# Optimization experiments

Hardware: AMD Instinct MI355X
Metric: run time of the kernel (lower is better)

## Reference

```python
import jax, jax.numpy as jnp
import numpy as np

N = 50000
IN_C = 128
HID = 128  # 2 * out_channels
OUT_C = 64
E = 800000


def setup_inputs() -> dict:
    key = jax.random.key(0)
    k1, k2, k3, k4, k5, k6 = jax.random.split(key, 6)
    x = jax.random.normal(k1, (N, IN_C), dtype=jnp.float32)
    edge_index = jax.random.randint(k2, (2, E), 0, N, dtype=jnp.int64)
    # Glorot init like PyG GCNConv
    W1 = jax.random.normal(k3, (IN_C, HID), dtype=jnp.float32) * np.sqrt(2.0 / (IN_C + HID))
    b1 = jnp.zeros((HID,), dtype=jnp.float32)
    W2 = jax.random.normal(k4, (HID, OUT_C), dtype=jnp.float32) * np.sqrt(2.0 / (HID + OUT_C))
    b2 = jnp.zeros((OUT_C,), dtype=jnp.float32)
    return {"x": x, "edge_index": edge_index, "W1": W1, "b1": b1, "W2": W2, "b2": b2}


def _gcn_norm(edge_index, num_nodes):
    # PyG gcn_norm with add_self_loops=True, edge_weight=1:
    # deg[i] = number of incoming edges to i (including self loop)
    # norm(e) = deg[src]^-0.5 * deg[dst]^-0.5
    loops = jnp.arange(num_nodes, dtype=edge_index.dtype)
    src = jnp.concatenate([edge_index[0], loops])
    dst = jnp.concatenate([edge_index[1], loops])
    deg = jax.ops.segment_sum(jnp.ones_like(dst, dtype=jnp.float32), dst,
                              num_segments=num_nodes)
    dinv = jnp.where(deg > 0, jax.lax.rsqrt(deg), 0.0)
    norm = dinv[src] * dinv[dst]
    return src, dst, norm


def _gcn_layer(x, W, b, src, dst, norm, num_nodes):
    h = x @ W                                    # [N, D_out] dense GEMM first (PyG order)
    msg = h[src] * norm[:, None]                 # gather + scale: [E+N, D_out]
    out = jax.ops.segment_sum(msg, dst, num_segments=num_nodes)  # scatter-add
    return out + b


def reference(x, edge_index, W1, b1, W2, b2):
    num_nodes = x.shape[0]
    # cached=True in the original: normalization computed once, reused by both convs
    src, dst, norm = _gcn_norm(edge_index, num_nodes)
    h = _gcn_layer(x, W1, b1, src, dst, norm, num_nodes)
    h = jax.nn.relu(h)
    out = _gcn_layer(h, W2, b2, src, dst, norm, num_nodes)
    return out
```

## Files before the change

### kernel.cpp

```cpp
#include <hip/hip_runtime.h>
#include <hip/hip_bf16.h>


typedef unsigned short ushort_t;
typedef __attribute__((ext_vector_type(8))) short bf16x8;
typedef __attribute__((ext_vector_type(4))) float f32x4;

__device__ __forceinline__ float blo(int v) {
    union { int i; float f; } u;
    u.i = v << 16;
    return u.f;
}

__device__ __forceinline__ float bhi(int v) {
    union { int i; float f; } u;
    u.i = v & 0xffff0000;
    return u.f;
}

__device__ __forceinline__ ushort_t f2bf(float f) {
    __hip_bfloat16 h = __float2bfloat16(f);
    return *reinterpret_cast<ushort_t*>(&h);
}

#define BMAX 512
#define CHUNK 2048
#define CAP 3072
#define NPH 8


__global__ __launch_bounds__(256) void gemm1bin_k(const float* __restrict__ X,
                                                  const float* __restrict__ W,
                                                  ushort_t* __restrict__ H,
                                                  const int* __restrict__ src,
                                                  const int* __restrict__ dst,
                                                  int* __restrict__ bucket_cursor,
                                                  int* __restrict__ binned,
                                                  int n, int E, int G1) {
    __shared__ __align__(16) char smem[52224];
    const int t = threadIdx.x;

    if ((int)blockIdx.x < G1) {
        ushort_t (*As)[136] = reinterpret_cast<ushort_t(*)[136]>(smem);
        ushort_t (*Bt)[136] = reinterpret_cast<ushort_t(*)[136]>(smem + 64 * 136 * 2);
        const int row0 = blockIdx.x * 64;
#pragma unroll
        for (int rep = 0; rep < 8; rep++) {
            int idx = rep * 1024 + t * 4;
            int r = idx >> 7, c = idx & 127;
            int gr = row0 + r;
            float4 v = make_float4(0.f, 0.f, 0.f, 0.f);
            if (gr < n) v = *reinterpret_cast<const float4*>(X + (size_t)gr * 128 + c);
            As[r][c + 0] = f2bf(v.x); As[r][c + 1] = f2bf(v.y);
            As[r][c + 2] = f2bf(v.z); As[r][c + 3] = f2bf(v.w);
        }
#pragma unroll
        for (int rep = 0; rep < 16; rep++) {
            int idx = rep * 1024 + t * 4;
            int k = idx >> 7, nn = idx & 127;
            float4 v = *reinterpret_cast<const float4*>(W + k * 128 + nn);
            Bt[nn + 0][k] = f2bf(v.x); Bt[nn + 1][k] = f2bf(v.y);
            Bt[nn + 2][k] = f2bf(v.z); Bt[nn + 3][k] = f2bf(v.w);
        }
        __syncthreads();
        const int lane = t & 63;
        const int wave = t >> 6;
        const int l15 = lane & 15;
        const int koff = (lane >> 4) * 8;
        f32x4 acc[8] = {};
#pragma unroll
        for (int ks = 0; ks < 4; ks++) {
            int kb = ks * 32 + koff;
            bf16x8 a = *reinterpret_cast<const bf16x8*>(&As[wave * 16 + l15][kb]);
#pragma unroll
            for (int tc = 0; tc < 8; tc++) {
                bf16x8 b = *reinterpret_cast<const bf16x8*>(&Bt[tc * 16 + l15][kb]);
                acc[tc] = __builtin_amdgcn_mfma_f32_16x16x32_bf16(a, b, acc[tc], 0, 0, 0);
            }
        }
        const int rbase = row0 + wave * 16 + (lane >> 4) * 4;
#pragma unroll
        for (int reg = 0; reg < 4; reg++) {
            int gr = rbase + reg;
            if (gr < n) {
#pragma unroll
                for (int tc = 0; tc < 8; tc++)
                    H[(size_t)gr * 128 + tc * 16 + l15] = f2bf(acc[tc][reg]);
            }
        }
    } else {
        int* lcnt = (int*)smem;
        int* lbase = lcnt + BMAX;
        int* lcur = lbase + BMAX;
        const int nchunks = (E + CHUNK - 1) / CHUNK;
        const int nbin = (int)gridDim.x - G1;
        for (int ch = (int)blockIdx.x - G1; ch < nchunks; ch += nbin) {
            int base = ch * CHUNK;
            int cnt = min(CHUNK, E - base);
            for (int i = t; i < BMAX; i += 256) lcnt[i] = 0;
            __syncthreads();
            for (int k = t; k < cnt; k += 256)
                atomicAdd(&lcnt[dst[base + k] >> 7], 1);
            __syncthreads();
            for (int i = t; i < BMAX; i += 256) {
                int c = lcnt[i];
                if (c) lbase[i] = atomicAdd(&bucket_cursor[i], c);
                lcur[i] = 0;
            }
            __syncthreads();
            for (int k = t; k < cnt; k += 256) {
                int d = dst[base + k];
                int b = d >> 7;
                int r = atomicAdd(&lcur[b], 1);
                int pos = lbase[b] + r;
                if (pos < CAP)
                    binned[b * CAP + pos] = (src[base + k] << 7) | (d & 127);
            }
            __syncthreads();
        }
    }
}

__global__ __launch_bounds__(256) void finalize_k(const int* __restrict__ binned,
                                                  const int* __restrict__ bucket_cursor,
                                                  float* __restrict__ dinv,
                                                  int2* __restrict__ row_range,
                                                  ushort_t* __restrict__ csr,
                                                  int N, int B) {
    __shared__ int cnt[128][NPH];
    __shared__ int sc[128];
    int b = blockIdx.x;
    int tid = threadIdx.x;
    int node0 = b << 7;
    int nn = min(128, N - node0);
    int e0 = b * CAP;
    int e1 = e0 + min(bucket_cursor[b], CAP);
    const int phw = (N + NPH - 1) / NPH;

    for (int i = tid; i < 128 * NPH; i += 256) ((int*)cnt)[i] = 0;
    __syncthreads();
    for (int k = e0 + tid; k < e1; k += 256) {
        int e = binned[k];
        int s = (int)((unsigned)e >> 7);
        atomicAdd(&cnt[e & 127][s / phw], 1);
    }
    __syncthreads();
    int deg = 0;
    int pre[NPH];
    if (tid < 128) {
#pragma unroll
        for (int p = 0; p < NPH; p++) { pre[p] = deg; deg += cnt[tid][p]; }
        sc[tid] = (tid < nn) ? deg : 0;
    }
    __syncthreads();
    for (int off = 1; off < 128; off <<= 1) {
        int t2 = 0;
        if (tid < 128 && tid >= off) t2 = sc[tid - off];
        __syncthreads();
        if (tid < 128) sc[tid] += t2;
        __syncthreads();
    }
    if (tid < nn) {
        int ex = sc[tid] - deg;
        int g = node0 + tid;
        dinv[g] = rsqrtf((float)deg + 1.0f);
        row_range[g] = make_int2(e0 + ex, e0 + ex + deg);
#pragma unroll
        for (int p = 0; p < NPH; p++) cnt[tid][p] = ex + pre[p];
    }
    __syncthreads();
    for (int k = e0 + tid; k < e1; k += 256) {
        int e = binned[k];
        int s = (int)((unsigned)e >> 7);
        int slot = atomicAdd(&cnt[e & 127][s / phw], 1);
        csr[e0 + slot] = (ushort_t)s;
    }
}


__global__ __launch_bounds__(256) void gemm2_k(const ushort_t* __restrict__ X,
                                               const float* __restrict__ W,
                                               const float* __restrict__ dinv,
                                               ushort_t* __restrict__ H, int n) {
    __shared__ ushort_t As[64][136];
    __shared__ ushort_t Bt[64][136];
    const int t = threadIdx.x;
    const int row0 = blockIdx.x * 64;
#pragma unroll
    for (int rep = 0; rep < 8; rep++) {
        int idx = rep * 1024 + t * 4;
        int r = idx >> 7, c = idx & 127;
        int gr = row0 + r;
        ushort4 v = make_ushort4(0, 0, 0, 0);
        if (gr < n) v = *reinterpret_cast<const ushort4*>(X + (size_t)gr * 128 + c);
        As[r][c + 0] = v.x; As[r][c + 1] = v.y; As[r][c + 2] = v.z; As[r][c + 3] = v.w;
    }
#pragma unroll
    for (int rep = 0; rep < 8; rep++) {
        int idx = rep * 1024 + t * 4;
        int k = idx >> 6, nn = idx & 63;
        float4 v = *reinterpret_cast<const float4*>(W + k * 64 + nn);
        Bt[nn + 0][k] = f2bf(v.x); Bt[nn + 1][k] = f2bf(v.y);
        Bt[nn + 2][k] = f2bf(v.z); Bt[nn + 3][k] = f2bf(v.w);
    }
    __syncthreads();
    const int lane = t & 63;
    const int wave = t >> 6;
    const int l15 = lane & 15;
    const int koff = (lane >> 4) * 8;
    f32x4 acc[4] = {};
#pragma unroll
    for (int ks = 0; ks < 4; ks++) {
        int kb = ks * 32 + koff;
        bf16x8 a = *reinterpret_cast<const bf16x8*>(&As[wave * 16 + l15][kb]);
#pragma unroll
        for (int tc = 0; tc < 4; tc++) {
            bf16x8 b = *reinterpret_cast<const bf16x8*>(&Bt[tc * 16 + l15][kb]);
            acc[tc] = __builtin_amdgcn_mfma_f32_16x16x32_bf16(a, b, acc[tc], 0, 0, 0);
        }
    }
    const int rbase = row0 + wave * 16 + (lane >> 4) * 4;
#pragma unroll
    for (int reg = 0; reg < 4; reg++) {
        int gr = rbase + reg;
        if (gr < n) {
            float dv = dinv[gr];
#pragma unroll
            for (int tc = 0; tc < 4; tc++)
                H[(size_t)gr * 64 + tc * 16 + l15] = f2bf(acc[tc][reg] * dv);
        }
    }
}

#define FMA8(VV, WT)                                                    \
    a0 = fmaf(blo((VV).x), (WT), a0); a1 = fmaf(bhi((VV).x), (WT), a1); \
    a2 = fmaf(blo((VV).y), (WT), a2); a3 = fmaf(bhi((VV).y), (WT), a3); \
    a4 = fmaf(blo((VV).z), (WT), a4); a5 = fmaf(bhi((VV).z), (WT), a5); \
    a6 = fmaf(blo((VV).w), (WT), a6); a7 = fmaf(bhi((VV).w), (WT), a7);


__global__ __launch_bounds__(256) void agg1_k(const ushort_t* __restrict__ h,
                                              const int2* __restrict__ row_range,
                                              const ushort_t* __restrict__ csr,
                                              const float* __restrict__ dinv,
                                              const float* __restrict__ bias,
                                              ushort_t* __restrict__ out, int n) {
    const int t = threadIdx.x;
    const int i = blockIdx.x * 16 + (t >> 4);
    if (i >= n) return;
    const int q = t & 15;
    const ushort_t* hq = h + 8 * q;
    float a0 = 0.f, a1 = 0.f, a2 = 0.f, a3 = 0.f;
    float a4 = 0.f, a5 = 0.f, a6 = 0.f, a7 = 0.f;
    const int2 rr = row_range[i];
    const int e = rr.y - 1;
    for (int j = rr.x; j < rr.y; j += 16) {
        int ss[16];
#pragma unroll
        for (int k = 0; k < 16; k++) ss[k] = (int)csr[min(j + k, e)];
        float ww[16];
#pragma unroll
        for (int k = 0; k < 16; k++) ww[k] = (j + k <= e) ? dinv[ss[k]] : 0.f;
#pragma unroll
        for (int k = 0; k < 16; k++) {
            int4 v = *reinterpret_cast<const int4*>(hq + (size_t)ss[k] * 128);
            FMA8(v, ww[k]);
        }
    }
    const float di = dinv[i];
    int4 sv = *reinterpret_cast<const int4*>(hq + (size_t)i * 128);
    FMA8(sv, di);
    float4 b0 = *reinterpret_cast<const float4*>(bias + 8 * q);
    float4 b1v = *reinterpret_cast<const float4*>(bias + 8 * q + 4);
    int4 o;
    o.x = (int)(((unsigned)f2bf(fmaxf(fmaf(di, a1, b0.y), 0.f)) << 16) | f2bf(fmaxf(fmaf(di, a0, b0.x), 0.f)));
    o.y = (int)(((unsigned)f2bf(fmaxf(fmaf(di, a3, b0.w), 0.f)) << 16) | f2bf(fmaxf(fmaf(di, a2, b0.z), 0.f)));
    o.z = (int)(((unsigned)f2bf(fmaxf(fmaf(di, a5, b1v.y), 0.f)) << 16) | f2bf(fmaxf(fmaf(di, a4, b1v.x), 0.f)));
    o.w = (int)(((unsigned)f2bf(fmaxf(fmaf(di, a7, b1v.w), 0.f)) << 16) | f2bf(fmaxf(fmaf(di, a6, b1v.z), 0.f)));
    *reinterpret_cast<int4*>(out + (size_t)i * 128 + 8 * q) = o;
}


__global__ __launch_bounds__(256) void agg2_k(const ushort_t* __restrict__ h,
                                              const int2* __restrict__ row_range,
                                              const ushort_t* __restrict__ csr,
                                              const float* __restrict__ dinv,
                                              const float* __restrict__ bias,
                                              float* __restrict__ out, int n) {
    const int t = threadIdx.x;
    const int i = blockIdx.x * 32 + (t >> 3);
    if (i >= n) return;
    const int q = t & 7;
    const ushort_t* hq = h + 8 * q;
    float a0 = 0.f, a1 = 0.f, a2 = 0.f, a3 = 0.f;
    float a4 = 0.f, a5 = 0.f, a6 = 0.f, a7 = 0.f;
    const int2 rr = row_range[i];
    const int e = rr.y - 1;
    for (int j = rr.x; j < rr.y; j += 16) {
        int ss[16];
#pragma unroll
        for (int k = 0; k < 16; k++) ss[k] = (int)csr[min(j + k, e)];
        float ww[16];
#pragma unroll
        for (int k = 0; k < 16; k++) ww[k] = (j + k <= e) ? 1.f : 0.f;
#pragma unroll
        for (int k = 0; k < 16; k++) {
            int4 v = *reinterpret_cast<const int4*>(hq + (size_t)ss[k] * 64);
            FMA8(v, ww[k]);
        }
    }
    int4 sv = *reinterpret_cast<const int4*>(hq + (size_t)i * 64);
    FMA8(sv, 1.f);
    const float di = dinv[i];
    float4 b0 = *reinterpret_cast<const float4*>(bias + 8 * q);
    float4 b1v = *reinterpret_cast<const float4*>(bias + 8 * q + 4);
    float4 o0 = make_float4(fmaf(di, a0, b0.x), fmaf(di, a1, b0.y),
                            fmaf(di, a2, b0.z), fmaf(di, a3, b0.w));
    float4 o1 = make_float4(fmaf(di, a4, b1v.x), fmaf(di, a5, b1v.y),
                            fmaf(di, a6, b1v.z), fmaf(di, a7, b1v.w));
    *reinterpret_cast<float4*>(out + (size_t)i * 64 + 8 * q) = o0;
    *reinterpret_cast<float4*>(out + (size_t)i * 64 + 8 * q + 4) = o1;
}


extern "C" void kernel_launch(void* const* d_in, const int* in_sizes, int n_in,
                              void* d_out, int out_size, void* d_ws, size_t ws_size,
                              hipStream_t stream) {
    const float* x   = (const float*)d_in[0];
    const int*   ei  = (const int*)d_in[1];
    const float* W1  = (const float*)d_in[2];
    const float* b1  = (const float*)d_in[3];
    const float* W2  = (const float*)d_in[4];
    const float* b2  = (const float*)d_in[5];
    float* out = (float*)d_out;

    const int N = in_sizes[0] / 128;
    const int E = in_sizes[1] / 2;
    const int B = (N + 127) >> 7;
    const int* src = ei;
    const int* dst = ei + E;

    char* p = (char*)d_ws;
    auto alloc = [&](size_t bytes) {
        char* q = p;
        p += (bytes + 255) & ~(size_t)255;
        return (void*)q;
    };
    int*      bucket_cursor = (int*)alloc((size_t)BMAX * 4);
    float*    dinv          = (float*)alloc((size_t)N * 4);
    int2*     row_range     = (int2*)alloc((size_t)N * 8);
    int*      binned        = (int*)alloc((size_t)B * CAP * 4);
    ushort_t* csr           = (ushort_t*)alloc(((size_t)B * CAP + 32) * 2);
    ushort_t* h1            = (ushort_t*)alloc((size_t)N * 128 * 2);
    ushort_t* agg1          = (ushort_t*)alloc((size_t)N * 128 * 2);
    ushort_t* h2            = h1;

    const int nchunks = (E + CHUNK - 1) / CHUNK;
    const int G1 = (N + 63) / 64;

    (void)hipMemsetAsync(bucket_cursor, 0, (size_t)B * 4, stream);
    gemm1bin_k<<<G1 + nchunks, 256, 0, stream>>>(x, W1, h1, src, dst,
                                                 bucket_cursor, binned, N, E, G1);
    finalize_k<<<B, 256, 0, stream>>>(binned, bucket_cursor, dinv, row_range, csr, N, B);

    agg1_k<<<(N + 15) / 16, 256, 0, stream>>>(h1, row_range, csr, dinv, b1, agg1, N);

    gemm2_k<<<(N + 63) / 64, 256, 0, stream>>>(agg1, W2, dinv, h2, N);
    agg2_k<<<(N + 31) / 32, 256, 0, stream>>>(h2, row_range, csr, dinv, b2, out, N);
}
```

Baseline: 185.6 us.

## Prescale layer-1 features by source dinv in finalize, drop per-edge dinv gather

The finalize kernel now multiplies each node's bf16 row of h1 by its own dinv after computing degrees, so agg1 no longer has to gather dinv[src] for every edge. Both aggregation kernels also replace the batched 16-wide index/weight prefetch with a simpler 8-wide unrolled loop. This removes one dependent random gather per edge in agg1, but adds a read-modify-write pass over h1 and an extra bf16 rounding step, and the smaller unroll may expose less memory-level parallelism.

```diff
diff --git a/kernel.cpp b/kernel.cpp
--- a/kernel.cpp
+++ b/kernel.cpp
@@ -21,6 +21,15 @@
 __device__ __forceinline__ ushort_t f2bf(float f) {
     __hip_bfloat16 h = __float2bfloat16(f);
     return *reinterpret_cast<ushort_t*>(&h);
+}
+
+__device__ __forceinline__ int4 scale8(int4 v, float s) {
+    int4 r;
+    r.x = (int)(((unsigned)f2bf(bhi(v.x) * s) << 16) | f2bf(blo(v.x) * s));
+    r.y = (int)(((unsigned)f2bf(bhi(v.y) * s) << 16) | f2bf(blo(v.y) * s));
+    r.z = (int)(((unsigned)f2bf(bhi(v.z) * s) << 16) | f2bf(blo(v.z) * s));
+    r.w = (int)(((unsigned)f2bf(bhi(v.w) * s) << 16) | f2bf(blo(v.w) * s));
+    return r;
 }
 
 #define BMAX 512
@@ -126,9 +135,11 @@
                                                   float* __restrict__ dinv,
                                                   int2* __restrict__ row_range,
                                                   ushort_t* __restrict__ csr,
+                                                  ushort_t* __restrict__ h1,
                                                   int N, int B) {
     __shared__ int cnt[128][NPH];
     __shared__ int sc[128];
+    __shared__ float sdv[128];
     int b = blockIdx.x;
     int tid = threadIdx.x;
     int node0 = b << 7;
@@ -160,13 +171,18 @@
         if (tid < 128) sc[tid] += t2;
         __syncthreads();
     }
-    if (tid < nn) {
-        int ex = sc[tid] - deg;
-        int g = node0 + tid;
-        dinv[g] = rsqrtf((float)deg + 1.0f);
-        row_range[g] = make_int2(e0 + ex, e0 + ex + deg);
-#pragma unroll
-        for (int p = 0; p < NPH; p++) cnt[tid][p] = ex + pre[p];
+    if (tid < 128) {
+        float dv = 0.f;
+        if (tid < nn) {
+            int ex = sc[tid] - deg;
+            int g = node0 + tid;
+            dv = rsqrtf((float)deg + 1.0f);
+            dinv[g] = dv;
+            row_range[g] = make_int2(e0 + ex, e0 + ex + deg);
+#pragma unroll
+            for (int p = 0; p < NPH; p++) cnt[tid][p] = ex + pre[p];
+        }
+        sdv[tid] = dv;
     }
     __syncthreads();
     for (int k = e0 + tid; k < e1; k += 256) {
@@ -174,6 +190,12 @@
         int s = (int)((unsigned)e >> 7);
         int slot = atomicAdd(&cnt[e & 127][s / phw], 1);
         csr[e0 + slot] = (ushort_t)s;
+    }
+    int4* h4 = reinterpret_cast<int4*>(h1);
+    for (int idx = tid; idx < nn * 16; idx += 256) {
+        int r = idx >> 4, c = idx & 15;
+        size_t off = (size_t)(node0 + r) * 16 + c;
+        h4[off] = scale8(h4[off], sdv[r]);
     }
 }
 
@@ -254,22 +276,19 @@
     float a4 = 0.f, a5 = 0.f, a6 = 0.f, a7 = 0.f;
     const int2 rr = row_range[i];
     const int e = rr.y - 1;
-    for (int j = rr.x; j < rr.y; j += 16) {
-        int ss[16];
-#pragma unroll
-        for (int k = 0; k < 16; k++) ss[k] = (int)csr[min(j + k, e)];
-        float ww[16];
-#pragma unroll
-        for (int k = 0; k < 16; k++) ww[k] = (j + k <= e) ? dinv[ss[k]] : 0.f;
-#pragma unroll
-        for (int k = 0; k < 16; k++) {
-            int4 v = *reinterpret_cast<const int4*>(hq + (size_t)ss[k] * 128);
-            FMA8(v, ww[k]);
+    for (int j = rr.x; j < rr.y; j += 8) {
+#pragma unroll
+        for (int k = 0; k < 8; k++) {
+            int jk = min(j + k, e);
+            int s = (int)csr[jk];
+            float w = (j + k <= e) ? 1.f : 0.f;
+            int4 v = *reinterpret_cast<const int4*>(hq + (size_t)s * 128);
+            FMA8(v, w);
         }
     }
     const float di = dinv[i];
     int4 sv = *reinterpret_cast<const int4*>(hq + (size_t)i * 128);
-    FMA8(sv, di);
+    FMA8(sv, 1.f);
     float4 b0 = *reinterpret_cast<const float4*>(bias + 8 * q);
     float4 b1v = *reinterpret_cast<const float4*>(bias + 8 * q + 4);
     int4 o;
@@ -296,17 +315,14 @@
     float a4 = 0.f, a5 = 0.f, a6 = 0.f, a7 = 0.f;
     const int2 rr = row_range[i];
     const int e = rr.y - 1;
-    for (int j = rr.x; j < rr.y; j += 16) {
-        int ss[16];
-#pragma unroll
-        for (int k = 0; k < 16; k++) ss[k] = (int)csr[min(j + k, e)];
-        float ww[16];
-#pragma unroll
-        for (int k = 0; k < 16; k++) ww[k] = (j + k <= e) ? 1.f : 0.f;
-#pragma unroll
-        for (int k = 0; k < 16; k++) {
-            int4 v = *reinterpret_cast<const int4*>(hq + (size_t)ss[k] * 64);
-            FMA8(v, ww[k]);
+    for (int j = rr.x; j < rr.y; j += 8) {
+#pragma unroll
+        for (int k = 0; k < 8; k++) {
+            int jk = min(j + k, e);
+            int s = (int)csr[jk];
+            float w = (j + k <= e) ? 1.f : 0.f;
+            int4 v = *reinterpret_cast<const int4*>(hq + (size_t)s * 64);
+            FMA8(v, w);
         }
     }
     int4 sv = *reinterpret_cast<const int4*>(hq + (size_t)i * 64);
@@ -361,7 +377,7 @@
     (void)hipMemsetAsync(bucket_cursor, 0, (size_t)B * 4, stream);
     gemm1bin_k<<<G1 + nchunks, 256, 0, stream>>>(x, W1, h1, src, dst,
                                                  bucket_cursor, binned, N, E, G1);
-    finalize_k<<<B, 256, 0, stream>>>(binned, bucket_cursor, dinv, row_range, csr, N, B);
+    finalize_k<<<B, 256, 0, stream>>>(binned, bucket_cursor, dinv, row_range, csr, h1, N, B);
 
     agg1_k<<<(N + 15) / 16, 256, 0, stream>>>(h1, row_range, csr, dinv, b1, agg1, N);
 
```

Result: faster. 181.4 us (-2.3%).
